# Kernel optimization log

Measured on AMD Instinct MI355X. Metric: run time of the kernel, lower is better.

The kernel has to match this reference:

```python
import jax, jax.numpy as jnp
import numpy as np

B, T, D, H = 512, 128, 128, 128
EPS = 1e-6


def setup_inputs() -> dict:
    key = jax.random.key(0)
    ks = jax.random.split(key, 16)
    def n(k, shape, s=0.05):
        return jax.random.normal(k, shape, dtype=jnp.float32) * s
    values = jax.random.normal(ks[0], (B, T, D), dtype=jnp.float32)
    masks = (jax.random.uniform(ks[1], (B, T, D)) > 0.3).astype(jnp.float32)
    deltas = jax.random.uniform(ks[2], (B, T, D), dtype=jnp.float32) * 5.0
    eye = jnp.eye(D, dtype=jnp.float32)
    Wth = n(ks[3], (H, D));            bth = jnp.zeros((H,), jnp.float32)
    Wtx = n(ks[4], (D, D)) * (1 - eye); btx = jnp.zeros((D,), jnp.float32)
    Whr = n(ks[5], (H, D));            bhr = jnp.zeros((D,), jnp.float32)
    Wfr = n(ks[6], (D, D)) * (1 - eye); bfr = jnp.zeros((D,), jnp.float32)
    Wwc = n(ks[7], (2 * D, D));        bwc = jnp.zeros((D,), jnp.float32)
    Wk = n(ks[8], (2 * D, 4 * H))      # LSTM input kernel
    Wr = n(ks[9], (H, 4 * H))          # LSTM recurrent kernel
    bl = jnp.zeros((4 * H,), jnp.float32)
    Wd = n(ks[10], (H, D));            bd = jnp.zeros((D,), jnp.float32)
    Wo = n(ks[11], (D, 1));            bo = jnp.zeros((1,), jnp.float32)
    return dict(values=values, masks=masks, deltas=deltas,
                Wth=Wth, bth=bth, Wtx=Wtx, btx=btx, Whr=Whr, bhr=bhr,
                Wfr=Wfr, bfr=bfr, Wwc=Wwc, bwc=bwc,
                Wk=Wk, Wr=Wr, bl=bl, Wd=Wd, bd=bd, Wo=Wo, bo=bo)


def reference(values, masks, deltas,
              Wth, bth, Wtx, btx, Whr, bhr, Wfr, bfr, Wwc, bwc,
              Wk, Wr, bl, Wd, bd, Wo, bo):
    # time-major sequences: [T, B, D]
    xs = jnp.moveaxis(values, 1, 0)
    ms = jnp.moveaxis(masks, 1, 0)
    ds = jnp.moveaxis(deltas, 1, 0)

    def step(carry, inp):
        h, c = carry
        x, m, d = inp
        gamma_h = jnp.exp(-jax.nn.relu(d @ Wth.T + bth))   # [B,H]
        h = h * gamma_h
        x_hat = h @ Whr + bhr                               # [B,D]
        denom = jnp.sum(m) + EPS                            # scalar (TF reduce_sum over all)
        loss = jnp.sum(jnp.abs(x - x_hat) * m / denom, axis=1)
        x_c = m * x + (1 - m) * x_hat
        z_hat = x_c @ Wfr.T + bfr
        loss += jnp.sum(jnp.abs(x - z_hat) * m / denom, axis=1)
        gamma_x = jnp.exp(-jax.nn.relu(d @ Wtx.T + btx))    # [B,D]
        beta = jnp.concatenate([gamma_x, m], axis=1) @ Wwc + bwc
        c_hat = beta * z_hat + (1 - beta) * x_hat
        loss += jnp.sum(jnp.abs(x - c_hat) * m / denom, axis=1)
        c_c = m * x + (1 - m) * c_hat                       # imputation at step t
        # LSTM cell (Keras gate order i,f,g,o; sigmoid/tanh)
        gates = jnp.concatenate([c_c, m], axis=1) @ Wk + h @ Wr + bl
        i, f, g, o = jnp.split(gates, 4, axis=1)
        c_new = jax.nn.sigmoid(f) * c + jax.nn.sigmoid(i) * jnp.tanh(g)
        h_new = jax.nn.sigmoid(o) * jnp.tanh(c_new)
        return (h_new, c_new), (c_c, loss)

    h0 = jnp.zeros((values.shape[0], H), jnp.float32)
    c0 = jnp.zeros((values.shape[0], H), jnp.float32)
    (h, _), (imps, losses) = jax.lax.scan(step, (h0, c0), (xs, ms, ds))
    imputations = jnp.moveaxis(imps, 0, 1)                  # [B,T,D]
    predictions = jax.nn.relu(h @ Wd + bd) @ Wo + bo        # [B,1]
    custom_loss = jnp.mean(jnp.moveaxis(losses, 0, 1), axis=1)  # [B]
    return predictions, imputations, custom_loss
```

## Files before the change

### kernel.cpp

```cpp
#include <hip/hip_runtime.h>
#include <hip/hip_bf16.h>

#define BB 512
#define TT 128
#define DD 128
#define HH 128
#define EPSV 1e-6f

typedef _Float16 f16x2 __attribute__((ext_vector_type(2)));

__device__ __forceinline__ float dot2f(unsigned a, unsigned b, float c) {
#if __has_builtin(__builtin_amdgcn_fdot2)
    return __builtin_amdgcn_fdot2(__builtin_bit_cast(f16x2, a),
                                  __builtin_bit_cast(f16x2, b), c, false);
#else
    f16x2 fa = __builtin_bit_cast(f16x2, a);
    f16x2 fb = __builtin_bit_cast(f16x2, b);
    return fmaf((float)fa.y, (float)fb.y, fmaf((float)fa.x, (float)fb.x, c));
#endif
}

__device__ __forceinline__ unsigned pkh(float a, float b) {
    f16x2 v; v.x = (_Float16)a; v.y = (_Float16)b;
    return __builtin_bit_cast(unsigned, v);
}

__device__ __forceinline__ float2 uph(unsigned u) {
    f16x2 v = __builtin_bit_cast(f16x2, u);
    return make_float2((float)v.x, (float)v.y);
}

__device__ __forceinline__ float bflo(unsigned u) { return __builtin_bit_cast(float, u << 16); }
__device__ __forceinline__ float bfhi(unsigned u) { return __builtin_bit_cast(float, u & 0xffff0000u); }

__device__ __forceinline__ float sigm(float x) { return 1.f / (1.f + __expf(-x)); }
__device__ __forceinline__ float tanhfast(float x) {
    float t = __expf(2.f * x);
    return 1.f - 2.f / (t + 1.f);
}

__global__ __launch_bounds__(256) void k_denom(const float* __restrict__ masks,
                                               float* __restrict__ invden) {
    int t = blockIdx.x;
    float s = 0.f;
    for (int idx = threadIdx.x; idx < BB * DD; idx += 256) {
        int b = idx >> 7, j = idx & 127;
        s += masks[((size_t)b * TT + t) * DD + j];
    }
    __shared__ float red[256];
    red[threadIdx.x] = s;
    __syncthreads();
    for (int off = 128; off > 0; off >>= 1) {
        if (threadIdx.x < off) red[threadIdx.x] += red[threadIdx.x + off];
        __syncthreads();
    }
    if (threadIdx.x == 0) invden[t] = 1.f / (red[0] + EPSV);
}

__global__ __launch_bounds__(256) void k_pack2(const float* __restrict__ Wk,
                                               const float* __restrict__ Wr,
                                               unsigned* __restrict__ wp2) {
    int idx = blockIdx.x * 256 + threadIdx.x;
    int c = idx >> 11;
    int t = (idx >> 2) & 511;
    int e = idx & 3;
    int i = c * 4 + e;
    int kq = t >> 6, n8 = t & 63;
    int kk2 = i >> 3, jn = i & 7;
    int k0 = kq * 48 + 2 * kk2;
    int n = n8 * 8 + jn;
    float w0, w1;
    {
        int k = k0;
        w0 = (k < 128) ? Wk[(size_t)k * 512 + n]
           : (k < 256) ? Wr[(size_t)(k - 128) * 512 + n]
                       : Wk[(size_t)(k - 128) * 512 + n];
        k = k0 + 1;
        w1 = (k < 128) ? Wk[(size_t)k * 512 + n]
           : (k < 256) ? Wr[(size_t)(k - 128) * 512 + n]
                       : Wk[(size_t)(k - 128) * 512 + n];
    }
    wp2[idx] = pkh(w0, w1);
}

__global__ __launch_bounds__(256) void k_pre(
    const float* __restrict__ masks, const float* __restrict__ deltas,
    const float* __restrict__ Wth, const float* __restrict__ bth,
    const float* __restrict__ Wtx, const float* __restrict__ btx,
    const float* __restrict__ Wwc, const float* __restrict__ bwc,
    __hip_bfloat16* __restrict__ gH, __hip_bfloat16* __restrict__ beta) {

    __shared__ __align__(16) float dT[32][128];
    __shared__ __align__(16) float mT[32][128];
    __shared__ __align__(16) float gx[32][128];

    const int tid = threadIdx.x;
    const int r0 = blockIdx.x * 32;

    {
        const float4* d4 = (const float4*)(deltas + (size_t)r0 * 128);
        const float4* m4 = (const float4*)(masks + (size_t)r0 * 128);
        float4* dT4 = (float4*)&dT[0][0];
        float4* mT4 = (float4*)&mT[0][0];
        for (int i = tid; i < 32 * 32; i += 256) { dT4[i] = d4[i]; mT4[i] = m4[i]; }
    }
    __syncthreads();

    {
        const int c = tid;
        const float* Wrow = (c < 128) ? (Wth + (size_t)c * DD) : (Wtx + (size_t)(c - 128) * DD);
        const float bias = (c < 128) ? bth[c] : btx[c - 128];
        float acc[32];
#pragma unroll
        for (int r = 0; r < 32; ++r) acc[r] = 0.f;
        for (int k0 = 0; k0 < 128; k0 += 4) {
            float4 w = *(const float4*)(Wrow + k0);
#pragma unroll
            for (int r = 0; r < 32; ++r) {
                float4 a = *(const float4*)&dT[r][k0];
                acc[r] = fmaf(a.x, w.x, fmaf(a.y, w.y, fmaf(a.z, w.z, fmaf(a.w, w.w, acc[r]))));
            }
        }
#pragma unroll
        for (int r = 0; r < 32; ++r) {
            float v = __expf(-fmaxf(acc[r] + bias, 0.f));
            if (c < 128) gH[(size_t)(r0 + r) * 128 + c] = __float2bfloat16(v);
            else         gx[r][c - 128] = v;
        }
    }
    __syncthreads();

    {
        const int c = tid & 127, kh = tid >> 7;
        float acc[32];
#pragma unroll
        for (int r = 0; r < 32; ++r) acc[r] = 0.f;
        const float (*A2)[128] = (kh == 0) ? (const float (*)[128])gx : (const float (*)[128])mT;
        const float* wc = Wwc + (size_t)(kh * 128) * DD + c;
        for (int kk = 0; kk < 128; kk += 4) {
            float w0 = wc[(kk + 0) * DD], w1 = wc[(kk + 1) * DD];
            float w2 = wc[(kk + 2) * DD], w3 = wc[(kk + 3) * DD];
#pragma unroll
            for (int r = 0; r < 32; ++r) {
                float4 a = *(const float4*)&A2[r][kk];
                acc[r] = fmaf(a.x, w0, fmaf(a.y, w1, fmaf(a.z, w2, fmaf(a.w, w3, acc[r]))));
            }
        }
        float (*bpartS)[128] = dT;
        if (kh == 1) {
#pragma unroll
            for (int r = 0; r < 32; ++r) bpartS[r][c] = acc[r];
        }
        __syncthreads();
        if (kh == 0) {
            const float bb = bwc[c];
#pragma unroll
            for (int r = 0; r < 32; ++r) {
                float v = acc[r] + bpartS[r][c] + bb;
                beta[(size_t)(r0 + r) * 128 + c] = __float2bfloat16(v);
            }
        }
    }
}

__global__ __launch_bounds__(512, 2) void k_rnn2(
    const float* __restrict__ values, const float* __restrict__ masks,
    const float* __restrict__ Whr, const float* __restrict__ bhr,
    const float* __restrict__ Wfr, const float* __restrict__ bfr,
    const float* __restrict__ bl,
    const float* __restrict__ Wd, const float* __restrict__ bd,
    const float* __restrict__ Wo, const float* __restrict__ bo,
    const float* __restrict__ invden,
    const __hip_bfloat16* __restrict__ gHws, const __hip_bfloat16* __restrict__ betws,
    const unsigned* __restrict__ wp2,
    float* __restrict__ out)
{
    const int tid = threadIdx.x;
    const int b0 = blockIdx.x * 2;

    __shared__ __align__(16) unsigned whr2[128][68];
    __shared__ __align__(16) unsigned wfr2[128][68];
    __shared__ __align__(16) unsigned ag2[2][192];
    __shared__ __align__(16) unsigned xc2[2][64];
    __shared__ __align__(16) float part[4][2][128];
    __shared__ __align__(16) float gp[8][2][512];
    __shared__ __align__(16) float cst[2][128];
    __shared__ float blS[512];
    __shared__ float invdS[128];
    __shared__ float bhrS[128], bfrS[128];
    __shared__ float slots[8];
    __shared__ float lossAcc[2];

    unsigned wr_[192];
    {
        const uint4* wp4 = (const uint4*)wp2;
#pragma unroll
        for (int c = 0; c < 48; ++c) {
            uint4 q = wp4[c * 512 + tid];
            wr_[c * 4 + 0] = q.x; wr_[c * 4 + 1] = q.y;
            wr_[c * 4 + 2] = q.z; wr_[c * 4 + 3] = q.w;
        }
    }
    for (int idx = tid; idx < 8192; idx += 512) {
        int k2 = idx >> 7, j = idx & 127;
        whr2[j][k2] = pkh(Whr[(size_t)(2 * k2) * DD + j], Whr[(size_t)(2 * k2 + 1) * DD + j]);
    }
    for (int idx = tid; idx < 8192; idx += 512) {
        int j = idx >> 6, k2 = idx & 63;
        float2 w = *(const float2*)&Wfr[(size_t)j * DD + 2 * k2];
        wfr2[j][k2] = pkh(w.x, w.y);
    }
    blS[tid] = bl[tid];
    if (tid < 128) { invdS[tid] = invden[tid]; bhrS[tid] = bhr[tid]; bfrS[tid] = bfr[tid]; }
    if (tid < 128) {
        int row = tid >> 6, j2 = tid & 63;
        ag2[row][64 + j2] = 0u;
        *(float2*)&cst[row][2 * j2] = make_float2(0.f, 0.f);
    }
    if (tid < 2) lossAcc[tid] = 0.f;

    const int prow = tid >> 6, pj2 = tid & 63;
    const int pj = tid & 127, pkq4 = tid >> 7;
    const int gkq = tid >> 6, gn8 = tid & 63;

    float2 px, pm;
    unsigned pbet = 0, pgh = 0;
    if (tid < 128) {
        size_t r2 = ((size_t)(b0 + prow) * TT + 0) * DD + 2 * pj2;
        px = *(const float2*)(values + r2);
        pm = *(const float2*)(masks + r2);
        pbet = *(const unsigned*)(betws + r2);
        pgh  = *(const unsigned*)(gHws + r2);
    }
    __syncthreads();

    float xhat0 = 0.f, xhat1 = 0.f;
    float cx0 = 0.f, cx1 = 0.f, cm0 = 0.f, cm1 = 0.f;
    unsigned cbet = 0;

    for (int t = 0; t < TT; ++t) {
        if (tid < 128) {
            cx0 = px.x; cx1 = px.y; cm0 = pm.x; cm1 = pm.y; cbet = pbet;
            float g0 = bflo(pgh), g1 = bfhi(pgh);
            float2 hv = uph(ag2[prow][64 + pj2]);
            ag2[prow][64 + pj2] = pkh(hv.x * g0, hv.y * g1);
            ag2[prow][128 + pj2] = pkh(cm0, cm1);
        }
        __syncthreads();

        {
            const unsigned* wrow = &whr2[pj][pkq4 * 16];
            uint4 w0 = *(const uint4*)(wrow + 0);
            uint4 w1 = *(const uint4*)(wrow + 4);
            uint4 w2 = *(const uint4*)(wrow + 8);
            uint4 w3 = *(const uint4*)(wrow + 12);
            float s0 = 0.f, s1 = 0.f;
#pragma unroll
            for (int row = 0; row < 2; ++row) {
                const unsigned* ha = &ag2[row][64 + pkq4 * 16];
                uint4 a0 = *(const uint4*)(ha + 0);
                uint4 a1 = *(const uint4*)(ha + 4);
                uint4 a2 = *(const uint4*)(ha + 8);
                uint4 a3 = *(const uint4*)(ha + 12);
                float s = 0.f;
                s = dot2f(a0.x, w0.x, s); s = dot2f(a0.y, w0.y, s);
                s = dot2f(a0.z, w0.z, s); s = dot2f(a0.w, w0.w, s);
                s = dot2f(a1.x, w1.x, s); s = dot2f(a1.y, w1.y, s);
                s = dot2f(a1.z, w1.z, s); s = dot2f(a1.w, w1.w, s);
                s = dot2f(a2.x, w2.x, s); s = dot2f(a2.y, w2.y, s);
                s = dot2f(a2.z, w2.z, s); s = dot2f(a2.w, w2.w, s);
                s = dot2f(a3.x, w3.x, s); s = dot2f(a3.y, w3.y, s);
                s = dot2f(a3.z, w3.z, s); s = dot2f(a3.w, w3.w, s);
                if (row == 0) s0 = s; else s1 = s;
            }
            part[pkq4][0][pj] = s0;
            part[pkq4][1][pj] = s1;
        }
        __syncthreads();

        if (tid < 128) {
            float2 p0 = *(const float2*)&part[0][prow][2 * pj2];
            float2 p1 = *(const float2*)&part[1][prow][2 * pj2];
            float2 p2 = *(const float2*)&part[2][prow][2 * pj2];
            float2 p3 = *(const float2*)&part[3][prow][2 * pj2];
            xhat0 = p0.x + p1.x + p2.x + p3.x + bhrS[2 * pj2];
            xhat1 = p0.y + p1.y + p2.y + p3.y + bhrS[2 * pj2 + 1];
            float xc0 = cm0 * cx0 + (1.f - cm0) * xhat0;
            float xc1 = cm1 * cx1 + (1.f - cm1) * xhat1;
            xc2[prow][pj2] = pkh(xc0, xc1);
            float l = fabsf(cx0 - xhat0) * cm0 + fabsf(cx1 - xhat1) * cm1;
#pragma unroll
            for (int off = 32; off; off >>= 1) l += __shfl_xor(l, off);
            if ((tid & 63) == 0) slots[prow] = l;
        }
        __syncthreads();

        {
            const unsigned* wrow = &wfr2[pj][pkq4 * 16];
            uint4 w0 = *(const uint4*)(wrow + 0);
            uint4 w1 = *(const uint4*)(wrow + 4);
            uint4 w2 = *(const uint4*)(wrow + 8);
            uint4 w3 = *(const uint4*)(wrow + 12);
            float s0 = 0.f, s1 = 0.f;
#pragma unroll
            for (int row = 0; row < 2; ++row) {
                const unsigned* xa = &xc2[row][pkq4 * 16];
                uint4 a0 = *(const uint4*)(xa + 0);
                uint4 a1 = *(const uint4*)(xa + 4);
                uint4 a2 = *(const uint4*)(xa + 8);
                uint4 a3 = *(const uint4*)(xa + 12);
                float s = 0.f;
                s = dot2f(a0.x, w0.x, s); s = dot2f(a0.y, w0.y, s);
                s = dot2f(a0.z, w0.z, s); s = dot2f(a0.w, w0.w, s);
                s = dot2f(a1.x, w1.x, s); s = dot2f(a1.y, w1.y, s);
                s = dot2f(a1.z, w1.z, s); s = dot2f(a1.w, w1.w, s);
                s = dot2f(a2.x, w2.x, s); s = dot2f(a2.y, w2.y, s);
                s = dot2f(a2.z, w2.z, s); s = dot2f(a2.w, w2.w, s);
                s = dot2f(a3.x, w3.x, s); s = dot2f(a3.y, w3.y, s);
                s = dot2f(a3.z, w3.z, s); s = dot2f(a3.w, w3.w, s);
                if (row == 0) s0 = s; else s1 = s;
            }
            part[pkq4][0][pj] = s0;
            part[pkq4][1][pj] = s1;
        }
        __syncthreads();

        if (tid < 128) {
            float2 p0 = *(const float2*)&part[0][prow][2 * pj2];
            float2 p1 = *(const float2*)&part[1][prow][2 * pj2];
            float2 p2 = *(const float2*)&part[2][prow][2 * pj2];
            float2 p3 = *(const float2*)&part[3][prow][2 * pj2];
            float z0 = p0.x + p1.x + p2.x + p3.x + bfrS[2 * pj2];
            float z1 = p0.y + p1.y + p2.y + p3.y + bfrS[2 * pj2 + 1];
            float be0 = bflo(cbet), be1 = bfhi(cbet);
            float ch0 = be0 * z0 + (1.f - be0) * xhat0;
            float ch1 = be1 * z1 + (1.f - be1) * xhat1;
            float l = (fabsf(cx0 - z0) + fabsf(cx0 - ch0)) * cm0
                    + (fabsf(cx1 - z1) + fabsf(cx1 - ch1)) * cm1;
            float cc0 = cm0 * cx0 + (1.f - cm0) * ch0;
            float cc1 = cm1 * cx1 + (1.f - cm1) * ch1;
            ag2[prow][pj2] = pkh(cc0, cc1);
            size_t r2 = ((size_t)(b0 + prow) * TT + t) * DD + 2 * pj2;
            *(float2*)&out[512 + r2] = make_float2(cc0, cc1);
#pragma unroll
            for (int off = 32; off; off >>= 1) l += __shfl_xor(l, off);
            if ((tid & 63) == 0) slots[2 + prow] = l;
        }
        __syncthreads();

        if (tid < 128) {
            int tc = (t + 1 < TT) ? t + 1 : TT - 1;
            size_t r2 = ((size_t)(b0 + prow) * TT + tc) * DD + 2 * pj2;
            px = *(const float2*)(values + r2);
            pm = *(const float2*)(masks + r2);
            pbet = *(const unsigned*)(betws + r2);
            pgh  = *(const unsigned*)(gHws + r2);
        }
        {
            float acc0[8], acc1[8];
#pragma unroll
            for (int j = 0; j < 8; ++j) { acc0[j] = 0.f; acc1[j] = 0.f; }
#pragma unroll
            for (int c = 0; c < 6; ++c) {
                uint4 qa = *(const uint4*)&ag2[0][gkq * 24 + c * 4];
                uint4 qb = *(const uint4*)&ag2[1][gkq * 24 + c * 4];
#define GSTEP(AC, BC, E)                                        \
                {                                               \
                    _Pragma("unroll")                           \
                    for (int j = 0; j < 8; ++j) {               \
                        unsigned w = wr_[(c * 4 + (E)) * 8 + j];\
                        acc0[j] = dot2f((AC), w, acc0[j]);      \
                        acc1[j] = dot2f((BC), w, acc1[j]);      \
                    }                                           \
                }
                GSTEP(qa.x, qb.x, 0)
                GSTEP(qa.y, qb.y, 1)
                GSTEP(qa.z, qb.z, 2)
                GSTEP(qa.w, qb.w, 3)
#undef GSTEP
            }
            *(float4*)&gp[gkq][0][gn8 * 8]     = make_float4(acc0[0], acc0[1], acc0[2], acc0[3]);
            *(float4*)&gp[gkq][0][gn8 * 8 + 4] = make_float4(acc0[4], acc0[5], acc0[6], acc0[7]);
            *(float4*)&gp[gkq][1][gn8 * 8]     = make_float4(acc1[0], acc1[1], acc1[2], acc1[3]);
            *(float4*)&gp[gkq][1][gn8 * 8 + 4] = make_float4(acc1[4], acc1[5], acc1[6], acc1[7]);
        }
        __syncthreads();

        if (tid < 128) {
            float2 gi = make_float2(blS[2 * pj2],       blS[2 * pj2 + 1]);
            float2 gf = make_float2(blS[128 + 2 * pj2], blS[128 + 2 * pj2 + 1]);
            float2 gg = make_float2(blS[256 + 2 * pj2], blS[256 + 2 * pj2 + 1]);
            float2 go = make_float2(blS[384 + 2 * pj2], blS[384 + 2 * pj2 + 1]);
#pragma unroll
            for (int kq = 0; kq < 8; ++kq) {
                float2 v;
                v = *(const float2*)&gp[kq][prow][2 * pj2];       gi.x += v.x; gi.y += v.y;
                v = *(const float2*)&gp[kq][prow][128 + 2 * pj2]; gf.x += v.x; gf.y += v.y;
                v = *(const float2*)&gp[kq][prow][256 + 2 * pj2]; gg.x += v.x; gg.y += v.y;
                v = *(const float2*)&gp[kq][prow][384 + 2 * pj2]; go.x += v.x; go.y += v.y;
            }
            float2 cv = *(const float2*)&cst[prow][2 * pj2];
            float cn0 = sigm(gf.x) * cv.x + sigm(gi.x) * tanhfast(gg.x);
            float cn1 = sigm(gf.y) * cv.y + sigm(gi.y) * tanhfast(gg.y);
            float hn0 = sigm(go.x) * tanhfast(cn0);
            float hn1 = sigm(go.y) * tanhfast(cn1);
            *(float2*)&cst[prow][2 * pj2] = make_float2(cn0, cn1);
            ag2[prow][64 + pj2] = pkh(hn0, hn1);
        }
        if (tid < 2) lossAcc[tid] += (slots[tid] + slots[2 + tid]) * invdS[t];
        __syncthreads();
    }

    if (tid < 256) {
        int row = tid >> 7, j = tid & 127;
        float acc = 0.f;
        for (int k2 = 0; k2 < 64; ++k2) {
            float2 hv = uph(ag2[row][64 + k2]);
            acc = fmaf(hv.x, Wd[(size_t)(2 * k2) * DD + j], acc);
            acc = fmaf(hv.y, Wd[(size_t)(2 * k2 + 1) * DD + j], acc);
        }
        float y = fmaxf(acc + bd[j], 0.f) * Wo[j];
#pragma unroll
        for (int off = 32; off; off >>= 1) y += __shfl_xor(y, off);
        if ((tid & 63) == 0) slots[tid >> 6] = y;
    }
    __syncthreads();
    if (tid < 2) {
        out[b0 + tid] = slots[2 * tid] + slots[2 * tid + 1] + bo[0];
        out[512 + (size_t)BB * TT * DD + b0 + tid] = lossAcc[tid] * (1.f / TT);
    }
}

extern "C" void kernel_launch(void* const* d_in, const int* in_sizes, int n_in,
                              void* d_out, int out_size, void* d_ws, size_t ws_size,
                              hipStream_t stream) {
    const float* values = (const float*)d_in[0];
    const float* masks  = (const float*)d_in[1];
    const float* deltas = (const float*)d_in[2];
    const float* Wth = (const float*)d_in[3];
    const float* bth = (const float*)d_in[4];
    const float* Wtx = (const float*)d_in[5];
    const float* btx = (const float*)d_in[6];
    const float* Whr = (const float*)d_in[7];
    const float* bhr = (const float*)d_in[8];
    const float* Wfr = (const float*)d_in[9];
    const float* bfr = (const float*)d_in[10];
    const float* Wwc = (const float*)d_in[11];
    const float* bwc = (const float*)d_in[12];
    const float* Wk  = (const float*)d_in[13];
    const float* Wr  = (const float*)d_in[14];
    const float* bl  = (const float*)d_in[15];
    const float* Wd  = (const float*)d_in[16];
    const float* bd  = (const float*)d_in[17];
    const float* Wo  = (const float*)d_in[18];
    const float* bo  = (const float*)d_in[19];
    float* out = (float*)d_out;

    char* ws = (char*)d_ws;
    float* invden        = (float*)ws;
    __hip_bfloat16* gH   = (__hip_bfloat16*)(ws + 512);
    __hip_bfloat16* beta = (__hip_bfloat16*)(ws + 512 + 16777216);
    unsigned* wp2        = (unsigned*)(ws + 512 + 2 * 16777216);

    k_denom<<<TT, 256, 0, stream>>>(masks, invden);
    k_pack2<<<384, 256, 0, stream>>>(Wk, Wr, wp2);
    k_pre<<<(BB * TT) / 32, 256, 0, stream>>>(masks, deltas, Wth, bth, Wtx, btx, Wwc, bwc, gH, beta);
    k_rnn2<<<BB / 2, 512, 0, stream>>>(values, masks, Whr, bhr, Wfr, bfr, bl,
                                       Wd, bd, Wo, bo, invden, gH, beta, wp2, out);
}
```

Baseline: 991.8 us.

## Rewrite recurrent kernel with 1024 threads and fp16 dot2 precompute

The recurrent kernel now runs 1024 threads per block. It re-partitions the x_hat, feature-regression and LSTM gate matvecs across 16 wavefronts, halves the per-thread register-held LSTM weights, double-buffers per-step inputs in shared memory, and fuses the gamma_h decay into the LSTM epilogue. The precompute kernel switches from fp32 FMAs to packed fp16 dot2 with weights pre-packed by the pack kernel, and the denominator reduction uses float4 loads. The aim is to shorten the serial per-step critical path and cut the precompute cost, at the price of extra fp16 rounding and more synchronisation per step.

```diff
diff --git a/kernel.cpp b/kernel.cpp
--- a/kernel.cpp
+++ b/kernel.cpp
@@ -8,8 +8,9 @@
 #define EPSV 1e-6f
 
 typedef _Float16 f16x2 __attribute__((ext_vector_type(2)));
-
-__device__ __forceinline__ float dot2f(unsigned a, unsigned b, float c) {
+typedef unsigned u32;
+
+__device__ __forceinline__ float dot2f(u32 a, u32 b, float c) {
 #if __has_builtin(__builtin_amdgcn_fdot2)
     return __builtin_amdgcn_fdot2(__builtin_bit_cast(f16x2, a),
                                   __builtin_bit_cast(f16x2, b), c, false);
@@ -20,19 +21,16 @@
 #endif
 }
 
-__device__ __forceinline__ unsigned pkh(float a, float b) {
+__device__ __forceinline__ u32 pkh(float a, float b) {
     f16x2 v; v.x = (_Float16)a; v.y = (_Float16)b;
-    return __builtin_bit_cast(unsigned, v);
-}
-
-__device__ __forceinline__ float2 uph(unsigned u) {
+    return __builtin_bit_cast(u32, v);
+}
+__device__ __forceinline__ float2 uph(u32 u) {
     f16x2 v = __builtin_bit_cast(f16x2, u);
     return make_float2((float)v.x, (float)v.y);
 }
-
-__device__ __forceinline__ float bflo(unsigned u) { return __builtin_bit_cast(float, u << 16); }
-__device__ __forceinline__ float bfhi(unsigned u) { return __builtin_bit_cast(float, u & 0xffff0000u); }
-
+__device__ __forceinline__ float bflo(u32 u) { return __builtin_bit_cast(float, u << 16); }
+__device__ __forceinline__ float bfhi(u32 u) { return __builtin_bit_cast(float, u & 0xffff0000u); }
 __device__ __forceinline__ float sigm(float x) { return 1.f / (1.f + __expf(-x)); }
 __device__ __forceinline__ float tanhfast(float x) {
     float t = __expf(2.f * x);
@@ -43,9 +41,10 @@
                                                float* __restrict__ invden) {
     int t = blockIdx.x;
     float s = 0.f;
-    for (int idx = threadIdx.x; idx < BB * DD; idx += 256) {
-        int b = idx >> 7, j = idx & 127;
-        s += masks[((size_t)b * TT + t) * DD + j];
+    for (int idx = threadIdx.x; idx < BB * 32; idx += 256) {
+        int b = idx >> 5, q = idx & 31;
+        float4 v = *(const float4*)(masks + ((size_t)b * TT + t) * DD + q * 4);
+        s += v.x + v.y + v.z + v.w;
     }
     __shared__ float red[256];
     red[threadIdx.x] = s;
@@ -59,111 +58,140 @@
 
 __global__ __launch_bounds__(256) void k_pack2(const float* __restrict__ Wk,
                                                const float* __restrict__ Wr,
-                                               unsigned* __restrict__ wp2) {
+                                               const float* __restrict__ Wth,
+                                               const float* __restrict__ Wtx,
+                                               const float* __restrict__ Wwc,
+                                               u32* __restrict__ wp2) {
     int idx = blockIdx.x * 256 + threadIdx.x;
-    int c = idx >> 11;
-    int t = (idx >> 2) & 511;
-    int e = idx & 3;
-    int i = c * 4 + e;
-    int kq = t >> 6, n8 = t & 63;
-    int kk2 = i >> 3, jn = i & 7;
-    int k0 = kq * 48 + 2 * kk2;
-    int n = n8 * 8 + jn;
-    float w0, w1;
-    {
-        int k = k0;
-        w0 = (k < 128) ? Wk[(size_t)k * 512 + n]
-           : (k < 256) ? Wr[(size_t)(k - 128) * 512 + n]
-                       : Wk[(size_t)(k - 128) * 512 + n];
-        k = k0 + 1;
-        w1 = (k < 128) ? Wk[(size_t)k * 512 + n]
-           : (k < 256) ? Wr[(size_t)(k - 128) * 512 + n]
-                       : Wk[(size_t)(k - 128) * 512 + n];
-    }
-    wp2[idx] = pkh(w0, w1);
-}
-
-__global__ __launch_bounds__(256) void k_pre(
+    if (idx < 98304) {
+        int c = idx & 3;
+        int t = (idx >> 2) & 1023;
+        int i = idx >> 12;
+        int kq = t >> 7, n4 = t & 127;
+        int k0 = 2 * (kq * 24 + i);
+        int n = n4 * 4 + c;
+        float w0, w1;
+        {
+            int k = k0;
+            w0 = (k < 128) ? Wk[(size_t)k * 512 + n]
+               : (k < 256) ? Wr[(size_t)(k - 128) * 512 + n]
+                           : Wk[(size_t)(k - 128) * 512 + n];
+            k = k0 + 1;
+            w1 = (k < 128) ? Wk[(size_t)k * 512 + n]
+               : (k < 256) ? Wr[(size_t)(k - 128) * 512 + n]
+                           : Wk[(size_t)(k - 128) * 512 + n];
+        }
+        wp2[idx] = pkh(w0, w1);
+    } else if (idx < 114688) {
+        int p = idx - 98304;
+        int k2 = p >> 8, c = p & 255;
+        const float* Wsrc = (c < 128) ? (Wth + (size_t)c * DD) : (Wtx + (size_t)(c - 128) * DD);
+        wp2[idx] = pkh(Wsrc[2 * k2], Wsrc[2 * k2 + 1]);
+    } else {
+        int p = idx - 114688;
+        int kh = p >> 13, k2 = (p >> 7) & 63, c = p & 127;
+        int r = kh * 128 + 2 * k2;
+        wp2[idx] = pkh(Wwc[(size_t)r * DD + c], Wwc[(size_t)(r + 1) * DD + c]);
+    }
+}
+
+__global__ __launch_bounds__(256) void k_pre2(
     const float* __restrict__ masks, const float* __restrict__ deltas,
-    const float* __restrict__ Wth, const float* __restrict__ bth,
-    const float* __restrict__ Wtx, const float* __restrict__ btx,
-    const float* __restrict__ Wwc, const float* __restrict__ bwc,
+    const float* __restrict__ bth, const float* __restrict__ btx,
+    const float* __restrict__ bwc,
+    const u32* __restrict__ wpre1, const u32* __restrict__ wpre2,
     __hip_bfloat16* __restrict__ gH, __hip_bfloat16* __restrict__ beta) {
 
-    __shared__ __align__(16) float dT[32][128];
-    __shared__ __align__(16) float mT[32][128];
-    __shared__ __align__(16) float gx[32][128];
+    __shared__ __align__(16) u32 dp[32][64];
+    __shared__ __align__(16) u32 mp[32][64];
+    __shared__ __align__(16) u32 gxp[32][64];
+    __shared__ __align__(16) float bpart[32][128];
 
     const int tid = threadIdx.x;
     const int r0 = blockIdx.x * 32;
 
-    {
-        const float4* d4 = (const float4*)(deltas + (size_t)r0 * 128);
-        const float4* m4 = (const float4*)(masks + (size_t)r0 * 128);
-        float4* dT4 = (float4*)&dT[0][0];
-        float4* mT4 = (float4*)&mT[0][0];
-        for (int i = tid; i < 32 * 32; i += 256) { dT4[i] = d4[i]; mT4[i] = m4[i]; }
+    for (int p = tid; p < 2048; p += 256) {
+        int r = p >> 6, k2 = p & 63;
+        float2 dv = *(const float2*)(deltas + (size_t)(r0 + r) * DD + 2 * k2);
+        float2 mv = *(const float2*)(masks + (size_t)(r0 + r) * DD + 2 * k2);
+        dp[r][k2] = pkh(dv.x, dv.y);
+        mp[r][k2] = pkh(mv.x, mv.y);
     }
     __syncthreads();
 
     {
         const int c = tid;
-        const float* Wrow = (c < 128) ? (Wth + (size_t)c * DD) : (Wtx + (size_t)(c - 128) * DD);
+        u32 wreg[64];
+#pragma unroll
+        for (int k2 = 0; k2 < 64; ++k2) wreg[k2] = wpre1[k2 * 256 + c];
         const float bias = (c < 128) ? bth[c] : btx[c - 128];
-        float acc[32];
-#pragma unroll
-        for (int r = 0; r < 32; ++r) acc[r] = 0.f;
-        for (int k0 = 0; k0 < 128; k0 += 4) {
-            float4 w = *(const float4*)(Wrow + k0);
-#pragma unroll
-            for (int r = 0; r < 32; ++r) {
-                float4 a = *(const float4*)&dT[r][k0];
-                acc[r] = fmaf(a.x, w.x, fmaf(a.y, w.y, fmaf(a.z, w.z, fmaf(a.w, w.w, acc[r]))));
-            }
-        }
-#pragma unroll
-        for (int r = 0; r < 32; ++r) {
-            float v = __expf(-fmaxf(acc[r] + bias, 0.f));
-            if (c < 128) gH[(size_t)(r0 + r) * 128 + c] = __float2bfloat16(v);
-            else         gx[r][c - 128] = v;
+        for (int half = 0; half < 2; ++half) {
+            float acc[16];
+#pragma unroll
+            for (int rr = 0; rr < 16; ++rr) acc[rr] = 0.f;
+#pragma unroll
+            for (int k4 = 0; k4 < 16; ++k4) {
+#pragma unroll
+                for (int rr = 0; rr < 16; ++rr) {
+                    uint4 dv = *(const uint4*)&dp[half * 16 + rr][k4 * 4];
+                    acc[rr] = dot2f(dv.x, wreg[k4 * 4 + 0], acc[rr]);
+                    acc[rr] = dot2f(dv.y, wreg[k4 * 4 + 1], acc[rr]);
+                    acc[rr] = dot2f(dv.z, wreg[k4 * 4 + 2], acc[rr]);
+                    acc[rr] = dot2f(dv.w, wreg[k4 * 4 + 3], acc[rr]);
+                }
+            }
+#pragma unroll
+            for (int rr = 0; rr < 16; ++rr) {
+                int r = half * 16 + rr;
+                float v = __expf(-fmaxf(acc[rr] + bias, 0.f));
+                if (c < 128) gH[(size_t)(r0 + r) * DD + c] = __float2bfloat16(v);
+                float vo = __shfl_xor(v, 1);
+                if (c >= 128 && !(c & 1)) gxp[r][(c - 128) >> 1] = pkh(v, vo);
+            }
         }
     }
     __syncthreads();
 
     {
-        const int c = tid & 127, kh = tid >> 7;
-        float acc[32];
-#pragma unroll
-        for (int r = 0; r < 32; ++r) acc[r] = 0.f;
-        const float (*A2)[128] = (kh == 0) ? (const float (*)[128])gx : (const float (*)[128])mT;
-        const float* wc = Wwc + (size_t)(kh * 128) * DD + c;
-        for (int kk = 0; kk < 128; kk += 4) {
-            float w0 = wc[(kk + 0) * DD], w1 = wc[(kk + 1) * DD];
-            float w2 = wc[(kk + 2) * DD], w3 = wc[(kk + 3) * DD];
-#pragma unroll
-            for (int r = 0; r < 32; ++r) {
-                float4 a = *(const float4*)&A2[r][kk];
-                acc[r] = fmaf(a.x, w0, fmaf(a.y, w1, fmaf(a.z, w2, fmaf(a.w, w3, acc[r]))));
-            }
-        }
-        float (*bpartS)[128] = dT;
-        if (kh == 1) {
-#pragma unroll
-            for (int r = 0; r < 32; ++r) bpartS[r][c] = acc[r];
-        }
-        __syncthreads();
-        if (kh == 0) {
-            const float bb = bwc[c];
-#pragma unroll
-            for (int r = 0; r < 32; ++r) {
-                float v = acc[r] + bpartS[r][c] + bb;
-                beta[(size_t)(r0 + r) * 128 + c] = __float2bfloat16(v);
-            }
-        }
-    }
-}
-
-__global__ __launch_bounds__(512, 2) void k_rnn2(
+        const int c2 = tid & 127, kh = tid >> 7;
+        u32 wreg[64];
+#pragma unroll
+        for (int k2 = 0; k2 < 64; ++k2) wreg[k2] = wpre2[kh * 8192 + k2 * 128 + c2];
+        const float bb = bwc[c2];
+        const u32 (*inp)[64] = kh ? mp : gxp;
+        for (int half = 0; half < 2; ++half) {
+            float acc[16];
+#pragma unroll
+            for (int rr = 0; rr < 16; ++rr) acc[rr] = 0.f;
+#pragma unroll
+            for (int k4 = 0; k4 < 16; ++k4) {
+#pragma unroll
+                for (int rr = 0; rr < 16; ++rr) {
+                    uint4 dv = *(const uint4*)&inp[half * 16 + rr][k4 * 4];
+                    acc[rr] = dot2f(dv.x, wreg[k4 * 4 + 0], acc[rr]);
+                    acc[rr] = dot2f(dv.y, wreg[k4 * 4 + 1], acc[rr]);
+                    acc[rr] = dot2f(dv.z, wreg[k4 * 4 + 2], acc[rr]);
+                    acc[rr] = dot2f(dv.w, wreg[k4 * 4 + 3], acc[rr]);
+                }
+            }
+            if (kh == 1) {
+#pragma unroll
+                for (int rr = 0; rr < 16; ++rr) bpart[half * 16 + rr][c2] = acc[rr];
+            }
+            __syncthreads();
+            if (kh == 0) {
+#pragma unroll
+                for (int rr = 0; rr < 16; ++rr) {
+                    int r = half * 16 + rr;
+                    beta[(size_t)(r0 + r) * DD + c2] =
+                        __float2bfloat16(acc[rr] + bpart[r][c2] + bb);
+                }
+            }
+        }
+    }
+}
+
+__global__ __launch_bounds__(1024, 4) void k_rnn3(
     const float* __restrict__ values, const float* __restrict__ masks,
     const float* __restrict__ Whr, const float* __restrict__ bhr,
     const float* __restrict__ Wfr, const float* __restrict__ bfr,
@@ -172,261 +200,232 @@
     const float* __restrict__ Wo, const float* __restrict__ bo,
     const float* __restrict__ invden,
     const __hip_bfloat16* __restrict__ gHws, const __hip_bfloat16* __restrict__ betws,
-    const unsigned* __restrict__ wp2,
+    const u32* __restrict__ wp2,
     float* __restrict__ out)
 {
     const int tid = threadIdx.x;
+    const int lane = tid & 63;
+    const int w = tid >> 6;
     const int b0 = blockIdx.x * 2;
 
-    __shared__ __align__(16) unsigned whr2[128][68];
-    __shared__ __align__(16) unsigned wfr2[128][68];
-    __shared__ __align__(16) unsigned ag2[2][192];
-    __shared__ __align__(16) unsigned xc2[2][64];
-    __shared__ __align__(16) float part[4][2][128];
+    __shared__ __align__(16) u32 whr2[128][68];
+    __shared__ __align__(16) u32 wfr2[128][68];
+    __shared__ __align__(16) u32 ag2[2][192];
+    __shared__ __align__(16) u32 xc2[2][64];
     __shared__ __align__(16) float gp[8][2][512];
-    __shared__ __align__(16) float cst[2][128];
+    __shared__ __align__(16) float xS[2][2][128], mS[2][2][128];
+    __shared__ __align__(16) u32 betS[2][2][64], ghS[2][2][64];
     __shared__ float blS[512];
-    __shared__ float invdS[128];
-    __shared__ float bhrS[128], bfrS[128];
-    __shared__ float slots[8];
+    __shared__ float invdS[128], bhrS[128], bfrS[128];
+    __shared__ float slots1[16], slots2[16];
     __shared__ float lossAcc[2];
-
-    unsigned wr_[192];
+    __shared__ float predS[4];
+
+    u32 wr_[96];
     {
         const uint4* wp4 = (const uint4*)wp2;
 #pragma unroll
-        for (int c = 0; c < 48; ++c) {
-            uint4 q = wp4[c * 512 + tid];
-            wr_[c * 4 + 0] = q.x; wr_[c * 4 + 1] = q.y;
-            wr_[c * 4 + 2] = q.z; wr_[c * 4 + 3] = q.w;
-        }
-    }
-    for (int idx = tid; idx < 8192; idx += 512) {
+        for (int i = 0; i < 24; ++i) {
+            uint4 q = wp4[i * 1024 + tid];
+            wr_[i * 4 + 0] = q.x; wr_[i * 4 + 1] = q.y;
+            wr_[i * 4 + 2] = q.z; wr_[i * 4 + 3] = q.w;
+        }
+    }
+    for (int idx = tid; idx < 8192; idx += 1024) {
         int k2 = idx >> 7, j = idx & 127;
         whr2[j][k2] = pkh(Whr[(size_t)(2 * k2) * DD + j], Whr[(size_t)(2 * k2 + 1) * DD + j]);
     }
-    for (int idx = tid; idx < 8192; idx += 512) {
+    for (int idx = tid; idx < 8192; idx += 1024) {
         int j = idx >> 6, k2 = idx & 63;
-        float2 w = *(const float2*)&Wfr[(size_t)j * DD + 2 * k2];
-        wfr2[j][k2] = pkh(w.x, w.y);
-    }
-    blS[tid] = bl[tid];
+        float2 wv = *(const float2*)&Wfr[(size_t)j * DD + 2 * k2];
+        wfr2[j][k2] = pkh(wv.x, wv.y);
+    }
+    if (tid < 512) blS[tid] = bl[tid];
     if (tid < 128) { invdS[tid] = invden[tid]; bhrS[tid] = bhr[tid]; bfrS[tid] = bfr[tid]; }
+    if (tid < 2) lossAcc[tid] = 0.f;
     if (tid < 128) {
-        int row = tid >> 6, j2 = tid & 63;
-        ag2[row][64 + j2] = 0u;
-        *(float2*)&cst[row][2 * j2] = make_float2(0.f, 0.f);
-    }
-    if (tid < 2) lossAcc[tid] = 0.f;
-
-    const int prow = tid >> 6, pj2 = tid & 63;
-    const int pj = tid & 127, pkq4 = tid >> 7;
-    const int gkq = tid >> 6, gn8 = tid & 63;
-
-    float2 px, pm;
-    unsigned pbet = 0, pgh = 0;
-    if (tid < 128) {
+        int prow = tid >> 6, pj2 = tid & 63;
         size_t r2 = ((size_t)(b0 + prow) * TT + 0) * DD + 2 * pj2;
-        px = *(const float2*)(values + r2);
-        pm = *(const float2*)(masks + r2);
-        pbet = *(const unsigned*)(betws + r2);
-        pgh  = *(const unsigned*)(gHws + r2);
-    }
+        float2 px = *(const float2*)(values + r2);
+        float2 pm = *(const float2*)(masks + r2);
+        u32 pb = *(const u32*)(betws + r2);
+        u32 pg = *(const u32*)(gHws + r2);
+        *(float2*)&xS[0][prow][2 * pj2] = px;
+        *(float2*)&mS[0][prow][2 * pj2] = pm;
+        betS[0][prow][pj2] = pb;
+        ghS[0][prow][pj2] = pg;
+        ag2[prow][128 + pj2] = pkh(pm.x, pm.y);
+        ag2[prow][64 + pj2] = 0u;
+    }
+    float cs = 0.f;
     __syncthreads();
 
-    float xhat0 = 0.f, xhat1 = 0.f;
-    float cx0 = 0.f, cx1 = 0.f, cm0 = 0.f, cm1 = 0.f;
-    unsigned cbet = 0;
+    const int grow = w >> 3, jb = w & 7;
+    const int jj = lane & 15, kq = lane >> 4;
+    const int j = jb * 16 + jj;
 
     for (int t = 0; t < TT; ++t) {
-        if (tid < 128) {
-            cx0 = px.x; cx1 = px.y; cm0 = pm.x; cm1 = pm.y; cbet = pbet;
-            float g0 = bflo(pgh), g1 = bfhi(pgh);
-            float2 hv = uph(ag2[prow][64 + pj2]);
-            ag2[prow][64 + pj2] = pkh(hv.x * g0, hv.y * g1);
-            ag2[prow][128 + pj2] = pkh(cm0, cm1);
+        const int cur = t & 1, nxt = cur ^ 1;
+        float xhat = 0.f;
+
+        {
+            const uint4* wrp = (const uint4*)&whr2[j][kq * 16];
+            const uint4* hap = (const uint4*)&ag2[grow][64 + kq * 16];
+            float s = 0.f;
+#pragma unroll
+            for (int c4 = 0; c4 < 4; ++c4) {
+                uint4 wv = wrp[c4]; uint4 av = hap[c4];
+                s = dot2f(av.x, wv.x, s); s = dot2f(av.y, wv.y, s);
+                s = dot2f(av.z, wv.z, s); s = dot2f(av.w, wv.w, s);
+            }
+            s += __shfl_xor(s, 16);
+            s += __shfl_xor(s, 32);
+            float xcv = 0.f;
+            if (lane < 16) {
+                xhat = s + bhrS[j];
+                float x = xS[cur][grow][j], m = mS[cur][grow][j];
+                xcv = m * x + (1.f - m) * xhat;
+                float l = fabsf(x - xhat) * m;
+                l += __shfl_xor(l, 8); l += __shfl_xor(l, 4);
+                l += __shfl_xor(l, 2); l += __shfl_xor(l, 1);
+                if (lane == 0) slots1[w] = l;
+            }
+            float xo = __shfl(xcv, 2 * (lane & 7));
+            float xo2 = __shfl(xcv, 2 * (lane & 7) + 1);
+            if (lane < 8) xc2[grow][jb * 8 + lane] = pkh(xo, xo2);
         }
         __syncthreads();
 
         {
-            const unsigned* wrow = &whr2[pj][pkq4 * 16];
-            uint4 w0 = *(const uint4*)(wrow + 0);
-            uint4 w1 = *(const uint4*)(wrow + 4);
-            uint4 w2 = *(const uint4*)(wrow + 8);
-            uint4 w3 = *(const uint4*)(wrow + 12);
-            float s0 = 0.f, s1 = 0.f;
-#pragma unroll
-            for (int row = 0; row < 2; ++row) {
-                const unsigned* ha = &ag2[row][64 + pkq4 * 16];
-                uint4 a0 = *(const uint4*)(ha + 0);
-                uint4 a1 = *(const uint4*)(ha + 4);
-                uint4 a2 = *(const uint4*)(ha + 8);
-                uint4 a3 = *(const uint4*)(ha + 12);
-                float s = 0.f;
-                s = dot2f(a0.x, w0.x, s); s = dot2f(a0.y, w0.y, s);
-                s = dot2f(a0.z, w0.z, s); s = dot2f(a0.w, w0.w, s);
-                s = dot2f(a1.x, w1.x, s); s = dot2f(a1.y, w1.y, s);
-                s = dot2f(a1.z, w1.z, s); s = dot2f(a1.w, w1.w, s);
-                s = dot2f(a2.x, w2.x, s); s = dot2f(a2.y, w2.y, s);
-                s = dot2f(a2.z, w2.z, s); s = dot2f(a2.w, w2.w, s);
-                s = dot2f(a3.x, w3.x, s); s = dot2f(a3.y, w3.y, s);
-                s = dot2f(a3.z, w3.z, s); s = dot2f(a3.w, w3.w, s);
-                if (row == 0) s0 = s; else s1 = s;
-            }
-            part[pkq4][0][pj] = s0;
-            part[pkq4][1][pj] = s1;
+            const uint4* wfp = (const uint4*)&wfr2[j][kq * 16];
+            const uint4* xap = (const uint4*)&xc2[grow][kq * 16];
+            float s = 0.f;
+#pragma unroll
+            for (int c4 = 0; c4 < 4; ++c4) {
+                uint4 wv = wfp[c4]; uint4 av = xap[c4];
+                s = dot2f(av.x, wv.x, s); s = dot2f(av.y, wv.y, s);
+                s = dot2f(av.z, wv.z, s); s = dot2f(av.w, wv.w, s);
+            }
+            s += __shfl_xor(s, 16);
+            s += __shfl_xor(s, 32);
+            float ccv = 0.f;
+            if (lane < 16) {
+                float z = s + bfrS[j];
+                u32 bu = betS[cur][grow][j >> 1];
+                float be = (j & 1) ? bfhi(bu) : bflo(bu);
+                float ch = be * z + (1.f - be) * xhat;
+                float x = xS[cur][grow][j], m = mS[cur][grow][j];
+                float l = (fabsf(x - z) + fabsf(x - ch)) * m;
+                ccv = m * x + (1.f - m) * ch;
+                out[512 + ((size_t)(b0 + grow) * TT + t) * DD + j] = ccv;
+                l += __shfl_xor(l, 8); l += __shfl_xor(l, 4);
+                l += __shfl_xor(l, 2); l += __shfl_xor(l, 1);
+                if (lane == 0) slots2[w] = l;
+            }
+            float co = __shfl(ccv, 2 * (lane & 7));
+            float co2 = __shfl(ccv, 2 * (lane & 7) + 1);
+            if (lane < 8) ag2[grow][jb * 8 + lane] = pkh(co, co2);
         }
         __syncthreads();
 
-        if (tid < 128) {
-            float2 p0 = *(const float2*)&part[0][prow][2 * pj2];
-            float2 p1 = *(const float2*)&part[1][prow][2 * pj2];
-            float2 p2 = *(const float2*)&part[2][prow][2 * pj2];
-            float2 p3 = *(const float2*)&part[3][prow][2 * pj2];
-            xhat0 = p0.x + p1.x + p2.x + p3.x + bhrS[2 * pj2];
-            xhat1 = p0.y + p1.y + p2.y + p3.y + bhrS[2 * pj2 + 1];
-            float xc0 = cm0 * cx0 + (1.f - cm0) * xhat0;
-            float xc1 = cm1 * cx1 + (1.f - cm1) * xhat1;
-            xc2[prow][pj2] = pkh(xc0, xc1);
-            float l = fabsf(cx0 - xhat0) * cm0 + fabsf(cx1 - xhat1) * cm1;
-#pragma unroll
-            for (int off = 32; off; off >>= 1) l += __shfl_xor(l, off);
-            if ((tid & 63) == 0) slots[prow] = l;
+        {
+            float2 px, pm; u32 pb = 0, pg = 0;
+            int prow = tid >> 6, pj2 = tid & 63;
+            if (tid < 128) {
+                int tc = (t + 1 < TT) ? t + 1 : TT - 1;
+                size_t r2 = ((size_t)(b0 + prow) * TT + tc) * DD + 2 * pj2;
+                px = *(const float2*)(values + r2);
+                pm = *(const float2*)(masks + r2);
+                pb = *(const u32*)(betws + r2);
+                pg = *(const u32*)(gHws + r2);
+            }
+            const int ckq = tid >> 7, cn4 = tid & 127;
+            float a0[4], a1[4];
+#pragma unroll
+            for (int c = 0; c < 4; ++c) { a0[c] = 0.f; a1[c] = 0.f; }
+            const uint4* g0 = (const uint4*)&ag2[0][ckq * 24];
+            const uint4* g1 = (const uint4*)&ag2[1][ckq * 24];
+#pragma unroll
+            for (int i = 0; i < 6; ++i) {
+                uint4 qa = g0[i]; uint4 qb = g1[i];
+#define GST(AV, BV, E)                                               \
+                {                                                    \
+                    _Pragma("unroll")                                \
+                    for (int c = 0; c < 4; ++c) {                    \
+                        u32 wv = wr_[(i * 4 + (E)) * 4 + c];         \
+                        a0[c] = dot2f((AV), wv, a0[c]);              \
+                        a1[c] = dot2f((BV), wv, a1[c]);              \
+                    }                                                \
+                }
+                GST(qa.x, qb.x, 0)
+                GST(qa.y, qb.y, 1)
+                GST(qa.z, qb.z, 2)
+                GST(qa.w, qb.w, 3)
+#undef GST
+            }
+            *(float4*)&gp[ckq][0][cn4 * 4] = make_float4(a0[0], a0[1], a0[2], a0[3]);
+            *(float4*)&gp[ckq][1][cn4 * 4] = make_float4(a1[0], a1[1], a1[2], a1[3]);
+            if (tid < 128) {
+                *(float2*)&xS[nxt][prow][2 * pj2] = px;
+                *(float2*)&mS[nxt][prow][2 * pj2] = pm;
+                betS[nxt][prow][pj2] = pb;
+                ghS[nxt][prow][pj2] = pg;
+            }
         }
         __syncthreads();
 
-        {
-            const unsigned* wrow = &wfr2[pj][pkq4 * 16];
-            uint4 w0 = *(const uint4*)(wrow + 0);
-            uint4 w1 = *(const uint4*)(wrow + 4);
-            uint4 w2 = *(const uint4*)(wrow + 8);
-            uint4 w3 = *(const uint4*)(wrow + 12);
-            float s0 = 0.f, s1 = 0.f;
-#pragma unroll
-            for (int row = 0; row < 2; ++row) {
-                const unsigned* xa = &xc2[row][pkq4 * 16];
-                uint4 a0 = *(const uint4*)(xa + 0);
-                uint4 a1 = *(const uint4*)(xa + 4);
-                uint4 a2 = *(const uint4*)(xa + 8);
-                uint4 a3 = *(const uint4*)(xa + 12);
-                float s = 0.f;
-                s = dot2f(a0.x, w0.x, s); s = dot2f(a0.y, w0.y, s);
-                s = dot2f(a0.z, w0.z, s); s = dot2f(a0.w, w0.w, s);
-                s = dot2f(a1.x, w1.x, s); s = dot2f(a1.y, w1.y, s);
-                s = dot2f(a1.z, w1.z, s); s = dot2f(a1.w, w1.w, s);
-                s = dot2f(a2.x, w2.x, s); s = dot2f(a2.y, w2.y, s);
-                s = dot2f(a2.z, w2.z, s); s = dot2f(a2.w, w2.w, s);
-                s = dot2f(a3.x, w3.x, s); s = dot2f(a3.y, w3.y, s);
-                s = dot2f(a3.z, w3.z, s); s = dot2f(a3.w, w3.w, s);
-                if (row == 0) s0 = s; else s1 = s;
-            }
-            part[pkq4][0][pj] = s0;
-            part[pkq4][1][pj] = s1;
+        if (tid < 256) {
+            const int drow = tid >> 7, hj = tid & 127;
+            float gi = blS[hj], gf = blS[128 + hj], gg = blS[256 + hj], go = blS[384 + hj];
+#pragma unroll
+            for (int k8 = 0; k8 < 8; ++k8) {
+                gi += gp[k8][drow][hj];
+                gf += gp[k8][drow][128 + hj];
+                gg += gp[k8][drow][256 + hj];
+                go += gp[k8][drow][384 + hj];
+            }
+            float cn = sigm(gf) * cs + sigm(gi) * tanhfast(gg);
+            float hn = sigm(go) * tanhfast(cn);
+            cs = cn;
+            float gam;
+            if (t == TT - 1) gam = 1.f;
+            else {
+                u32 gu = ghS[nxt][drow][hj >> 1];
+                gam = (hj & 1) ? bfhi(gu) : bflo(gu);
+            }
+            float hd = hn * gam;
+            float ho = __shfl_xor(hd, 1);
+            if (!(hj & 1)) {
+                ag2[drow][64 + (hj >> 1)] = pkh(hd, ho);
+                float2 mv = *(const float2*)&mS[nxt][drow][hj];
+                ag2[drow][128 + (hj >> 1)] = pkh(mv.x, mv.y);
+            }
+        }
+        if (tid < 2) {
+            float l = 0.f;
+#pragma unroll
+            for (int k8 = 0; k8 < 8; ++k8) l += slots1[tid * 8 + k8] + slots2[tid * 8 + k8];
+            lossAcc[tid] += l * invdS[t];
         }
         __syncthreads();
-
-        if (tid < 128) {
-            float2 p0 = *(const float2*)&part[0][prow][2 * pj2];
-            float2 p1 = *(const float2*)&part[1][prow][2 * pj2];
-            float2 p2 = *(const float2*)&part[2][prow][2 * pj2];
-            float2 p3 = *(const float2*)&part[3][prow][2 * pj2];
-            float z0 = p0.x + p1.x + p2.x + p3.x + bfrS[2 * pj2];
-            float z1 = p0.y + p1.y + p2.y + p3.y + bfrS[2 * pj2 + 1];
-            float be0 = bflo(cbet), be1 = bfhi(cbet);
-            float ch0 = be0 * z0 + (1.f - be0) * xhat0;
-            float ch1 = be1 * z1 + (1.f - be1) * xhat1;
-            float l = (fabsf(cx0 - z0) + fabsf(cx0 - ch0)) * cm0
-                    + (fabsf(cx1 - z1) + fabsf(cx1 - ch1)) * cm1;
-            float cc0 = cm0 * cx0 + (1.f - cm0) * ch0;
-            float cc1 = cm1 * cx1 + (1.f - cm1) * ch1;
-            ag2[prow][pj2] = pkh(cc0, cc1);
-            size_t r2 = ((size_t)(b0 + prow) * TT + t) * DD + 2 * pj2;
-            *(float2*)&out[512 + r2] = make_float2(cc0, cc1);
-#pragma unroll
-            for (int off = 32; off; off >>= 1) l += __shfl_xor(l, off);
-            if ((tid & 63) == 0) slots[2 + prow] = l;
-        }
-        __syncthreads();
-
-        if (tid < 128) {
-            int tc = (t + 1 < TT) ? t + 1 : TT - 1;
-            size_t r2 = ((size_t)(b0 + prow) * TT + tc) * DD + 2 * pj2;
-            px = *(const float2*)(values + r2);
-            pm = *(const float2*)(masks + r2);
-            pbet = *(const unsigned*)(betws + r2);
-            pgh  = *(const unsigned*)(gHws + r2);
-        }
-        {
-            float acc0[8], acc1[8];
-#pragma unroll
-            for (int j = 0; j < 8; ++j) { acc0[j] = 0.f; acc1[j] = 0.f; }
-#pragma unroll
-            for (int c = 0; c < 6; ++c) {
-                uint4 qa = *(const uint4*)&ag2[0][gkq * 24 + c * 4];
-                uint4 qb = *(const uint4*)&ag2[1][gkq * 24 + c * 4];
-#define GSTEP(AC, BC, E)                                        \
-                {                                               \
-                    _Pragma("unroll")                           \
-                    for (int j = 0; j < 8; ++j) {               \
-                        unsigned w = wr_[(c * 4 + (E)) * 8 + j];\
-                        acc0[j] = dot2f((AC), w, acc0[j]);      \
-                        acc1[j] = dot2f((BC), w, acc1[j]);      \
-                    }                                           \
-                }
-                GSTEP(qa.x, qb.x, 0)
-                GSTEP(qa.y, qb.y, 1)
-                GSTEP(qa.z, qb.z, 2)
-                GSTEP(qa.w, qb.w, 3)
-#undef GSTEP
-            }
-            *(float4*)&gp[gkq][0][gn8 * 8]     = make_float4(acc0[0], acc0[1], acc0[2], acc0[3]);
-            *(float4*)&gp[gkq][0][gn8 * 8 + 4] = make_float4(acc0[4], acc0[5], acc0[6], acc0[7]);
-            *(float4*)&gp[gkq][1][gn8 * 8]     = make_float4(acc1[0], acc1[1], acc1[2], acc1[3]);
-            *(float4*)&gp[gkq][1][gn8 * 8 + 4] = make_float4(acc1[4], acc1[5], acc1[6], acc1[7]);
-        }
-        __syncthreads();
-
-        if (tid < 128) {
-            float2 gi = make_float2(blS[2 * pj2],       blS[2 * pj2 + 1]);
-            float2 gf = make_float2(blS[128 + 2 * pj2], blS[128 + 2 * pj2 + 1]);
-            float2 gg = make_float2(blS[256 + 2 * pj2], blS[256 + 2 * pj2 + 1]);
-            float2 go = make_float2(blS[384 + 2 * pj2], blS[384 + 2 * pj2 + 1]);
-#pragma unroll
-            for (int kq = 0; kq < 8; ++kq) {
-                float2 v;
-                v = *(const float2*)&gp[kq][prow][2 * pj2];       gi.x += v.x; gi.y += v.y;
-                v = *(const float2*)&gp[kq][prow][128 + 2 * pj2]; gf.x += v.x; gf.y += v.y;
-                v = *(const float2*)&gp[kq][prow][256 + 2 * pj2]; gg.x += v.x; gg.y += v.y;
-                v = *(const float2*)&gp[kq][prow][384 + 2 * pj2]; go.x += v.x; go.y += v.y;
-            }
-            float2 cv = *(const float2*)&cst[prow][2 * pj2];
-            float cn0 = sigm(gf.x) * cv.x + sigm(gi.x) * tanhfast(gg.x);
-            float cn1 = sigm(gf.y) * cv.y + sigm(gi.y) * tanhfast(gg.y);
-            float hn0 = sigm(go.x) * tanhfast(cn0);
-            float hn1 = sigm(go.y) * tanhfast(cn1);
-            *(float2*)&cst[prow][2 * pj2] = make_float2(cn0, cn1);
-            ag2[prow][64 + pj2] = pkh(hn0, hn1);
-        }
-        if (tid < 2) lossAcc[tid] += (slots[tid] + slots[2 + tid]) * invdS[t];
-        __syncthreads();
     }
 
     if (tid < 256) {
-        int row = tid >> 7, j = tid & 127;
+        int row = tid >> 7, jd = tid & 127;
         float acc = 0.f;
         for (int k2 = 0; k2 < 64; ++k2) {
             float2 hv = uph(ag2[row][64 + k2]);
-            acc = fmaf(hv.x, Wd[(size_t)(2 * k2) * DD + j], acc);
-            acc = fmaf(hv.y, Wd[(size_t)(2 * k2 + 1) * DD + j], acc);
-        }
-        float y = fmaxf(acc + bd[j], 0.f) * Wo[j];
+            acc = fmaf(hv.x, Wd[(size_t)(2 * k2) * DD + jd], acc);
+            acc = fmaf(hv.y, Wd[(size_t)(2 * k2 + 1) * DD + jd], acc);
+        }
+        float y = fmaxf(acc + bd[jd], 0.f) * Wo[jd];
 #pragma unroll
         for (int off = 32; off; off >>= 1) y += __shfl_xor(y, off);
-        if ((tid & 63) == 0) slots[tid >> 6] = y;
+        if (lane == 0) predS[tid >> 6] = y;
     }
     __syncthreads();
     if (tid < 2) {
-        out[b0 + tid] = slots[2 * tid] + slots[2 * tid + 1] + bo[0];
+        out[b0 + tid] = predS[2 * tid] + predS[2 * tid + 1] + bo[0];
         out[512 + (size_t)BB * TT * DD + b0 + tid] = lossAcc[tid] * (1.f / TT);
     }
 }
@@ -460,11 +459,14 @@
     float* invden        = (float*)ws;
     __hip_bfloat16* gH   = (__hip_bfloat16*)(ws + 512);
     __hip_bfloat16* beta = (__hip_bfloat16*)(ws + 512 + 16777216);
-    unsigned* wp2        = (unsigned*)(ws + 512 + 2 * 16777216);
+    u32* wp2             = (u32*)(ws + 512 + 2 * 16777216);
+    const u32* wpre1     = wp2 + 98304;
+    const u32* wpre2     = wp2 + 114688;
 
     k_denom<<<TT, 256, 0, stream>>>(masks, invden);
-    k_pack2<<<384, 256, 0, stream>>>(Wk, Wr, wp2);
-    k_pre<<<(BB * TT) / 32, 256, 0, stream>>>(masks, deltas, Wth, bth, Wtx, btx, Wwc, bwc, gH, beta);
-    k_rnn2<<<BB / 2, 512, 0, stream>>>(values, masks, Whr, bhr, Wfr, bfr, bl,
-                                       Wd, bd, Wo, bo, invden, gH, beta, wp2, out);
-}
+    k_pack2<<<512, 256, 0, stream>>>(Wk, Wr, Wth, Wtx, Wwc, wp2);
+    k_pre2<<<(BB * TT) / 32, 256, 0, stream>>>(masks, deltas, bth, btx, bwc,
+                                               wpre1, wpre2, gH, beta);
+    k_rnn3<<<BB / 2, 1024, 0, stream>>>(values, masks, Whr, bhr, Wfr, bfr, bl,
+                                        Wd, bd, Wo, bo, invden, gH, beta, wp2, out);
+}
```

Result: slower. 3.017 ms (+204.2%).
